# Kernel tuning notes

Measured on AMD Instinct MI355X. Metric: run time of the kernel, lower is better.

The kernel has to match this reference:

```python
import jax, jax.numpy as jnp
import numpy as np

B, C, T, H, NCLS = 512, 22, 1000, 64, 4


def setup_inputs() -> dict:
    key = jax.random.key(0)
    ks = jax.random.split(key, 8)
    s_ih = 1.0 / np.sqrt(H)
    x = jax.random.normal(ks[0], (B, C, T), dtype=jnp.float32)
    # PyTorch LSTM params: gate order [i, f, g, o], each of size H
    W_ih = jax.random.uniform(ks[1], (4 * H, C), minval=-s_ih, maxval=s_ih, dtype=jnp.float32)
    W_hh = jax.random.uniform(ks[2], (4 * H, H), minval=-s_ih, maxval=s_ih, dtype=jnp.float32)
    b_ih = jax.random.uniform(ks[3], (4 * H,), minval=-s_ih, maxval=s_ih, dtype=jnp.float32)
    b_hh = jax.random.uniform(ks[4], (4 * H,), minval=-s_ih, maxval=s_ih, dtype=jnp.float32)
    s_fc = 1.0 / np.sqrt(H * T)
    W_fc = jax.random.uniform(ks[5], (NCLS, H * T), minval=-s_fc, maxval=s_fc, dtype=jnp.float32)
    b_fc = jax.random.uniform(ks[6], (NCLS,), minval=-s_fc, maxval=s_fc, dtype=jnp.float32)
    return {"x": x, "W_ih": W_ih, "W_hh": W_hh, "b_ih": b_ih, "b_hh": b_hh,
            "W_fc": W_fc, "b_fc": b_fc}


def _lstm(xs, W_ih, W_hh, b_ih, b_hh):
    # xs: [B, T, C] -> outputs [B, T, H]
    b = xs.shape[0]
    # precompute input projections for all timesteps: [T, B, 4H]
    x_proj = jnp.einsum('btc,gc->tbg', xs, W_ih) + (b_ih + b_hh)
    h0 = jnp.zeros((b, W_hh.shape[1]), xs.dtype)
    c0 = jnp.zeros_like(h0)

    def step(carry, xp):
        h, c = carry
        gates = xp + h @ W_hh.T  # [B, 4H]
        i, f, g, o = jnp.split(gates, 4, axis=-1)
        i = jax.nn.sigmoid(i)
        f = jax.nn.sigmoid(f)
        g = jnp.tanh(g)
        o = jax.nn.sigmoid(o)
        c = f * c + i * g
        h = o * jnp.tanh(c)
        return (h, c), h

    _, hs = jax.lax.scan(step, (h0, c0), x_proj)  # hs: [T, B, H]
    return jnp.transpose(hs, (1, 0, 2))  # [B, T, H]


def reference(x, W_ih, W_hh, b_ih, b_hh, W_fc, b_fc):
    xs = jnp.transpose(x, (0, 2, 1))  # [B, T, C]  (permute(0,2,1))
    hs = _lstm(xs, W_ih, W_hh, b_ih, b_hh)  # [B, T, H]
    flat = hs.reshape(hs.shape[0], -1)  # [B, T*H], time-major per row
    logits = flat @ W_fc.T + b_fc  # [B, 4]
    return jax.nn.softmax(logits, axis=1)
```

## Files before the change

### kernel.cpp

```cpp
#include <hip/hip_runtime.h>

#define BB   512
#define CC   22
#define TT   1000
#define HH   64
#define NCLS 4
#define TC   250
#define NCHUNK (TT / TC)
#define XROW 12

typedef _Float16 f16;
typedef __attribute__((ext_vector_type(2))) _Float16 h2;

__device__ __forceinline__ float sigm(float x) {
    return 1.0f / (1.0f + __expf(-x));
}
__device__ __forceinline__ float tanh_(float x) {
    float e = __expf(-2.0f * fabsf(x));
    float r = (1.0f - e) / (1.0f + e);
    return copysignf(r, x);
}

__device__ __forceinline__ h2 u2h(unsigned u) {
    union { unsigned u; h2 h; } c; c.u = u; return c.h;
}
__device__ __forceinline__ unsigned h2u(h2 h) {
    union { unsigned u; h2 h; } c; c.h = h; return c.u;
}

__global__
__attribute__((amdgpu_flat_work_group_size(64, 64), amdgpu_waves_per_eu(1, 1)))
void lstm_wave(
    const float* __restrict__ x,
    const float* __restrict__ W_ih,
    const float* __restrict__ W_hh,
    const float* __restrict__ b_ih,
    const float* __restrict__ b_hh,
    const float* __restrict__ W_fc,
    const float* __restrict__ b_fc,
    float* __restrict__ out)
{
    __shared__ __align__(16) h2  xs[TC][XROW];
    __shared__ __align__(16) f16 hbuf[HH];

    const int lane = threadIdx.x;
    const int r    = blockIdx.x;

    unsigned whh[4][32];
    unsigned wih[4][11];
    float bias[4];
    #pragma unroll
    for (int g = 0; g < 4; ++g) {
        const int row = g * HH + lane;
        const float* wr = W_hh + row * HH;
        #pragma unroll
        for (int k = 0; k < 32; ++k)
            whh[g][k] = h2u(h2{(f16)wr[2 * k], (f16)wr[2 * k + 1]});
        const float* wi = W_ih + row * CC;
        #pragma unroll
        for (int k = 0; k < 11; ++k)
            wih[g][k] = h2u(h2{(f16)wi[2 * k], (f16)wi[2 * k + 1]});
        bias[g] = b_ih[row] + b_hh[row];
    }

    hbuf[lane] = (f16)0.0f;
    float c = 0.0f;
    float fc0 = 0.f, fc1 = 0.f, fc2 = 0.f, fc3 = 0.f;
    const float* p0 = W_fc + 0 * (TT * HH) + lane;
    const float* p1 = W_fc + 1 * (TT * HH) + lane;
    const float* p2 = W_fc + 2 * (TT * HH) + lane;
    const float* p3 = W_fc + 3 * (TT * HH) + lane;
    const float* xrow = x + (size_t)r * (CC * TT);

    for (int chunk = 0; chunk < NCHUNK; ++chunk) {
        for (int tb = 0; tb < TC; tb += 64) {
            const int t = tb + lane;
            if (t < TC) {
                const float* gx = xrow + chunk * TC + t;
                union { h2 h[XROW]; uint4 q[3]; } U;
                #pragma unroll
                for (int k = 0; k < 11; ++k)
                    U.h[k] = h2{(f16)gx[(2 * k) * TT], (f16)gx[(2 * k + 1) * TT]};
                U.h[11] = h2{(f16)0.0f, (f16)0.0f};
                uint4* dst = (uint4*)&xs[t][0];
                dst[0] = U.q[0]; dst[1] = U.q[1]; dst[2] = U.q[2];
            }
        }

        for (int tt = 0; tt < TC; ++tt) {
            union { uint4 q[8]; h2 h[32]; } H;
            const uint4* hr = (const uint4*)hbuf;
            #pragma unroll
            for (int i = 0; i < 8; ++i) H.q[i] = hr[i];

            union { uint4 q[3]; h2 h[XROW]; } X;
            const uint4* xr = (const uint4*)&xs[tt][0];
            X.q[0] = xr[0]; X.q[1] = xr[1]; X.q[2] = xr[2];

            float w0 = *p0, w1 = *p1, w2 = *p2, w3 = *p3;
            p0 += HH; p1 += HH; p2 += HH; p3 += HH;

            float a0 = bias[0], a1 = bias[1], a2 = bias[2], a3 = bias[3];
            #pragma unroll
            for (int k = 0; k < 11; ++k) {
                a0 = __builtin_amdgcn_fdot2(X.h[k], u2h(wih[0][k]), a0, false);
                a1 = __builtin_amdgcn_fdot2(X.h[k], u2h(wih[1][k]), a1, false);
                a2 = __builtin_amdgcn_fdot2(X.h[k], u2h(wih[2][k]), a2, false);
                a3 = __builtin_amdgcn_fdot2(X.h[k], u2h(wih[3][k]), a3, false);
            }
            #pragma unroll
            for (int k = 0; k < 32; ++k) {
                a0 = __builtin_amdgcn_fdot2(H.h[k], u2h(whh[0][k]), a0, false);
                a1 = __builtin_amdgcn_fdot2(H.h[k], u2h(whh[1][k]), a1, false);
                a2 = __builtin_amdgcn_fdot2(H.h[k], u2h(whh[2][k]), a2, false);
                a3 = __builtin_amdgcn_fdot2(H.h[k], u2h(whh[3][k]), a3, false);
            }

            float iv = sigm(a0), fv = sigm(a1), gv = tanh_(a2), ov = sigm(a3);
            c = fv * c + iv * gv;
            float h = ov * tanh_(c);

            fc0 += h * w0; fc1 += h * w1; fc2 += h * w2; fc3 += h * w3;

            hbuf[lane] = (f16)h;
        }
    }

    #pragma unroll
    for (int off = 32; off; off >>= 1) {
        fc0 += __shfl_down(fc0, off);
        fc1 += __shfl_down(fc1, off);
        fc2 += __shfl_down(fc2, off);
        fc3 += __shfl_down(fc3, off);
    }
    if (lane == 0) {
        float l0 = fc0 + b_fc[0], l1 = fc1 + b_fc[1];
        float l2 = fc2 + b_fc[2], l3 = fc3 + b_fc[3];
        float m  = fmaxf(fmaxf(l0, l1), fmaxf(l2, l3));
        float e0 = __expf(l0 - m), e1 = __expf(l1 - m);
        float e2 = __expf(l2 - m), e3 = __expf(l3 - m);
        float s  = e0 + e1 + e2 + e3;
        float4 o; o.x = e0 / s; o.y = e1 / s; o.z = e2 / s; o.w = e3 / s;
        *(float4*)(out + r * NCLS) = o;
    }
}

extern "C" void kernel_launch(void* const* d_in, const int* in_sizes, int n_in,
                              void* d_out, int out_size, void* d_ws, size_t ws_size,
                              hipStream_t stream) {
    const float* x    = (const float*)d_in[0];
    const float* W_ih = (const float*)d_in[1];
    const float* W_hh = (const float*)d_in[2];
    const float* b_ih = (const float*)d_in[3];
    const float* b_hh = (const float*)d_in[4];
    const float* W_fc = (const float*)d_in[5];
    const float* b_fc = (const float*)d_in[6];
    float* out = (float*)d_out;

    lstm_wave<<<BB, 64, 0, stream>>>(x, W_ih, W_hh, b_ih, b_hh, W_fc, b_fc, out);
}
```

Measured before the change: 696.7 us.

## Use MFMA for LSTM recurrence and split FC+softmax into separate kernel

Replaces per-lane fdot2 gate computation with 16x16x32 f16 MFMA ops over weights held in registers, with x padded to 32 channels. Hidden states are buffered in an LDS ring and flushed to a global workspace. A second kernel then performs the FC projection and softmax. This removes the per-step W_fc loads from the serial loop but adds large global write/read traffic, and MFMA work is padded, with only 16 of 64 lane outputs used.

```diff
diff --git a/kernel.cpp b/kernel.cpp
--- a/kernel.cpp
+++ b/kernel.cpp
@@ -5,137 +5,173 @@
 #define TT   1000
 #define HH   64
 #define NCLS 4
-#define TC   250
+#define TC   200
 #define NCHUNK (TT / TC)
-#define XROW 12
+#define RING 40
 
 typedef _Float16 f16;
-typedef __attribute__((ext_vector_type(2))) _Float16 h2;
+typedef __attribute__((ext_vector_type(8))) _Float16 f16x8;
+typedef __attribute__((ext_vector_type(4))) float    f32x4;
 
-__device__ __forceinline__ float sigm(float x) {
-    return 1.0f / (1.0f + __expf(-x));
-}
+union F8U { f16x8 v; uint4 u; f16 h[8]; };
+
+__device__ __forceinline__ float sigm(float x) { return 1.0f / (1.0f + __expf(-x)); }
 __device__ __forceinline__ float tanh_(float x) {
     float e = __expf(-2.0f * fabsf(x));
     float r = (1.0f - e) / (1.0f + e);
     return copysignf(r, x);
 }
 
-__device__ __forceinline__ h2 u2h(unsigned u) {
-    union { unsigned u; h2 h; } c; c.u = u; return c.h;
-}
-__device__ __forceinline__ unsigned h2u(h2 h) {
-    union { unsigned u; h2 h; } c; c.h = h; return c.u;
-}
-
 __global__
 __attribute__((amdgpu_flat_work_group_size(64, 64), amdgpu_waves_per_eu(1, 1)))
-void lstm_wave(
+void lstm_mfma1(
     const float* __restrict__ x,
     const float* __restrict__ W_ih,
     const float* __restrict__ W_hh,
     const float* __restrict__ b_ih,
     const float* __restrict__ b_hh,
+    f16* __restrict__ hglob)
+{
+    __shared__ __align__(16) f16 xs[TC * 32];
+    __shared__ __align__(16) f16 hring[RING * HH];
+
+    const int lane = threadIdx.x;
+    const int q    = lane >> 4;
+    const int c    = lane & 15;
+    const int r    = blockIdx.x;
+
+    f16x8 Bw0[16], Bw1[16], Bw2[16];
+    float bias_s[16];
+    #pragma unroll
+    for (int n = 0; n < 16; ++n) {
+        const int g = 16 * n + c;
+        F8U a, b, cc;
+        const float* wr = W_hh + g * HH + 8 * q;
+        #pragma unroll
+        for (int j = 0; j < 8; ++j) { a.h[j] = (f16)wr[j]; b.h[j] = (f16)wr[32 + j]; }
+        #pragma unroll
+        for (int j = 0; j < 8; ++j) {
+            const int k = 8 * q + j;
+            cc.h[j] = (k < CC) ? (f16)W_ih[g * CC + k] : (f16)0.f;
+        }
+        Bw0[n] = a.v; Bw1[n] = b.v; Bw2[n] = cc.v;
+        bias_s[n] = b_ih[g] + b_hh[g];
+    }
+
+    if (lane < 16) {
+        #pragma unroll
+        for (int j = 0; j < 4; ++j) hring[(RING - 1) * HH + 16 * j + c] = (f16)0.f;
+    }
+    float cst[4] = {0.f, 0.f, 0.f, 0.f};
+    const float* xrow = x + (size_t)r * (CC * TT);
+    f16* hout = hglob + (size_t)r * (TT * HH);
+    int sprev = RING - 1, scur = 0;
+
+    for (int chunk = 0; chunk < NCHUNK; ++chunk) {
+        for (int t0 = 0; t0 < TC; t0 += 64) {
+            const int t = t0 + lane;
+            if (t < TC) {
+                const float* gx = xrow + chunk * TC + t;
+                F8U u[4];
+                #pragma unroll
+                for (int k = 0; k < 32; ++k)
+                    u[k >> 3].h[k & 7] = (k < CC) ? (f16)gx[k * TT] : (f16)0.f;
+                uint4* dst = (uint4*)&xs[t * 32];
+                dst[0] = u[0].u; dst[1] = u[1].u; dst[2] = u[2].u; dst[3] = u[3].u;
+            }
+        }
+
+        for (int tt = 0; tt < TC; ++tt) {
+            F8U Ax;  Ax.u  = *(const uint4*)&xs[tt * 32 + 8 * q];
+            F8U Ah0; Ah0.u = *(const uint4*)&hring[sprev * HH + 8 * q];
+            F8U Ah1; Ah1.u = *(const uint4*)&hring[sprev * HH + 32 + 8 * q];
+
+            const f32x4 z = {0.f, 0.f, 0.f, 0.f};
+            f32x4 acc[16];
+            #pragma unroll
+            for (int n = 0; n < 16; ++n)
+                acc[n] = __builtin_amdgcn_mfma_f32_16x16x32_f16(Ax.v, Bw2[n], z, 0, 0, 0);
+            #pragma unroll
+            for (int n = 0; n < 16; ++n)
+                acc[n] = __builtin_amdgcn_mfma_f32_16x16x32_f16(Ah0.v, Bw0[n], acc[n], 0, 0, 0);
+            #pragma unroll
+            for (int n = 0; n < 16; ++n)
+                acc[n] = __builtin_amdgcn_mfma_f32_16x16x32_f16(Ah1.v, Bw1[n], acc[n], 0, 0, 0);
+
+            #pragma unroll
+            for (int j = 0; j < 4; ++j) {
+                float iv = sigm (acc[j][0]      + bias_s[j]);
+                float fv = sigm (acc[4 + j][0]  + bias_s[4 + j]);
+                float gv = tanh_(acc[8 + j][0]  + bias_s[8 + j]);
+                float ov = sigm (acc[12 + j][0] + bias_s[12 + j]);
+                cst[j] = fv * cst[j] + iv * gv;
+                float h = ov * tanh_(cst[j]);
+                if (lane < 16) hring[scur * HH + 16 * j + c] = (f16)h;
+            }
+
+            if (scur == RING - 1) {
+                const int t0g = chunk * TC + tt - (RING - 1);
+                #pragma unroll
+                for (int j = 0; j < 5; ++j) {
+                    uint4 v = *(const uint4*)&hring[512 * j + 8 * lane];
+                    *(uint4*)&hout[(size_t)t0g * HH + 512 * j + 8 * lane] = v;
+                }
+            }
+            sprev = scur;
+            scur  = (scur + 1 == RING) ? 0 : scur + 1;
+        }
+    }
+}
+
+__global__ __launch_bounds__(256) void fc_softmax(
+    const f16*  __restrict__ hglob,
     const float* __restrict__ W_fc,
     const float* __restrict__ b_fc,
     float* __restrict__ out)
 {
-    __shared__ __align__(16) h2  xs[TC][XROW];
-    __shared__ __align__(16) f16 hbuf[HH];
+    const int w    = threadIdx.x >> 6;
+    const int lane = threadIdx.x & 63;
+    const int r    = blockIdx.x * 4 + w;
 
-    const int lane = threadIdx.x;
-    const int r    = blockIdx.x;
+    const f16* hr = hglob + (size_t)r * (TT * HH);
+    float a0 = 0.f, a1 = 0.f, a2 = 0.f, a3 = 0.f;
 
-    unsigned whh[4][32];
-    unsigned wih[4][11];
-    float bias[4];
-    #pragma unroll
-    for (int g = 0; g < 4; ++g) {
-        const int row = g * HH + lane;
-        const float* wr = W_hh + row * HH;
+    for (int i = 0; i < (TT * HH) / 512; ++i) {
+        const int k = i * 512 + lane * 8;
+        F8U hv; hv.u = *(const uint4*)&hr[k];
+        float hf[8];
         #pragma unroll
-        for (int k = 0; k < 32; ++k)
-            whh[g][k] = h2u(h2{(f16)wr[2 * k], (f16)wr[2 * k + 1]});
-        const float* wi = W_ih + row * CC;
-        #pragma unroll
-        for (int k = 0; k < 11; ++k)
-            wih[g][k] = h2u(h2{(f16)wi[2 * k], (f16)wi[2 * k + 1]});
-        bias[g] = b_ih[row] + b_hh[row];
-    }
+        for (int j = 0; j < 8; ++j) hf[j] = (float)hv.h[j];
 
-    hbuf[lane] = (f16)0.0f;
-    float c = 0.0f;
-    float fc0 = 0.f, fc1 = 0.f, fc2 = 0.f, fc3 = 0.f;
-    const float* p0 = W_fc + 0 * (TT * HH) + lane;
-    const float* p1 = W_fc + 1 * (TT * HH) + lane;
-    const float* p2 = W_fc + 2 * (TT * HH) + lane;
-    const float* p3 = W_fc + 3 * (TT * HH) + lane;
-    const float* xrow = x + (size_t)r * (CC * TT);
+        const float* w0 = W_fc + 0 * (TT * HH) + k;
+        const float* w1 = W_fc + 1 * (TT * HH) + k;
+        const float* w2 = W_fc + 2 * (TT * HH) + k;
+        const float* w3 = W_fc + 3 * (TT * HH) + k;
+        float4 v0a = *(const float4*)w0, v0b = *(const float4*)(w0 + 4);
+        float4 v1a = *(const float4*)w1, v1b = *(const float4*)(w1 + 4);
+        float4 v2a = *(const float4*)w2, v2b = *(const float4*)(w2 + 4);
+        float4 v3a = *(const float4*)w3, v3b = *(const float4*)(w3 + 4);
 
-    for (int chunk = 0; chunk < NCHUNK; ++chunk) {
-        for (int tb = 0; tb < TC; tb += 64) {
-            const int t = tb + lane;
-            if (t < TC) {
-                const float* gx = xrow + chunk * TC + t;
-                union { h2 h[XROW]; uint4 q[3]; } U;
-                #pragma unroll
-                for (int k = 0; k < 11; ++k)
-                    U.h[k] = h2{(f16)gx[(2 * k) * TT], (f16)gx[(2 * k + 1) * TT]};
-                U.h[11] = h2{(f16)0.0f, (f16)0.0f};
-                uint4* dst = (uint4*)&xs[t][0];
-                dst[0] = U.q[0]; dst[1] = U.q[1]; dst[2] = U.q[2];
-            }
-        }
-
-        for (int tt = 0; tt < TC; ++tt) {
-            union { uint4 q[8]; h2 h[32]; } H;
-            const uint4* hr = (const uint4*)hbuf;
-            #pragma unroll
-            for (int i = 0; i < 8; ++i) H.q[i] = hr[i];
-
-            union { uint4 q[3]; h2 h[XROW]; } X;
-            const uint4* xr = (const uint4*)&xs[tt][0];
-            X.q[0] = xr[0]; X.q[1] = xr[1]; X.q[2] = xr[2];
-
-            float w0 = *p0, w1 = *p1, w2 = *p2, w3 = *p3;
-            p0 += HH; p1 += HH; p2 += HH; p3 += HH;
-
-            float a0 = bias[0], a1 = bias[1], a2 = bias[2], a3 = bias[3];
-            #pragma unroll
-            for (int k = 0; k < 11; ++k) {
-                a0 = __builtin_amdgcn_fdot2(X.h[k], u2h(wih[0][k]), a0, false);
-                a1 = __builtin_amdgcn_fdot2(X.h[k], u2h(wih[1][k]), a1, false);
-                a2 = __builtin_amdgcn_fdot2(X.h[k], u2h(wih[2][k]), a2, false);
-                a3 = __builtin_amdgcn_fdot2(X.h[k], u2h(wih[3][k]), a3, false);
-            }
-            #pragma unroll
-            for (int k = 0; k < 32; ++k) {
-                a0 = __builtin_amdgcn_fdot2(H.h[k], u2h(whh[0][k]), a0, false);
-                a1 = __builtin_amdgcn_fdot2(H.h[k], u2h(whh[1][k]), a1, false);
-                a2 = __builtin_amdgcn_fdot2(H.h[k], u2h(whh[2][k]), a2, false);
-                a3 = __builtin_amdgcn_fdot2(H.h[k], u2h(whh[3][k]), a3, false);
-            }
-
-            float iv = sigm(a0), fv = sigm(a1), gv = tanh_(a2), ov = sigm(a3);
-            c = fv * c + iv * gv;
-            float h = ov * tanh_(c);
-
-            fc0 += h * w0; fc1 += h * w1; fc2 += h * w2; fc3 += h * w3;
-
-            hbuf[lane] = (f16)h;
-        }
+        a0 += hf[0]*v0a.x + hf[1]*v0a.y + hf[2]*v0a.z + hf[3]*v0a.w
+            + hf[4]*v0b.x + hf[5]*v0b.y + hf[6]*v0b.z + hf[7]*v0b.w;
+        a1 += hf[0]*v1a.x + hf[1]*v1a.y + hf[2]*v1a.z + hf[3]*v1a.w
+            + hf[4]*v1b.x + hf[5]*v1b.y + hf[6]*v1b.z + hf[7]*v1b.w;
+        a2 += hf[0]*v2a.x + hf[1]*v2a.y + hf[2]*v2a.z + hf[3]*v2a.w
+            + hf[4]*v2b.x + hf[5]*v2b.y + hf[6]*v2b.z + hf[7]*v2b.w;
+        a3 += hf[0]*v3a.x + hf[1]*v3a.y + hf[2]*v3a.z + hf[3]*v3a.w
+            + hf[4]*v3b.x + hf[5]*v3b.y + hf[6]*v3b.z + hf[7]*v3b.w;
     }
 
     #pragma unroll
     for (int off = 32; off; off >>= 1) {
-        fc0 += __shfl_down(fc0, off);
-        fc1 += __shfl_down(fc1, off);
-        fc2 += __shfl_down(fc2, off);
-        fc3 += __shfl_down(fc3, off);
+        a0 += __shfl_down(a0, off);
+        a1 += __shfl_down(a1, off);
+        a2 += __shfl_down(a2, off);
+        a3 += __shfl_down(a3, off);
     }
     if (lane == 0) {
-        float l0 = fc0 + b_fc[0], l1 = fc1 + b_fc[1];
-        float l2 = fc2 + b_fc[2], l3 = fc3 + b_fc[3];
+        float l0 = a0 + b_fc[0], l1 = a1 + b_fc[1];
+        float l2 = a2 + b_fc[2], l3 = a3 + b_fc[3];
         float m  = fmaxf(fmaxf(l0, l1), fmaxf(l2, l3));
         float e0 = __expf(l0 - m), e1 = __expf(l1 - m);
         float e2 = __expf(l2 - m), e3 = __expf(l3 - m);
@@ -156,6 +192,8 @@
     const float* W_fc = (const float*)d_in[5];
     const float* b_fc = (const float*)d_in[6];
     float* out = (float*)d_out;
+    f16*  hglob = (f16*)d_ws;
 
-    lstm_wave<<<BB, 64, 0, stream>>>(x, W_ih, W_hh, b_ih, b_hh, W_fc, b_fc, out);
+    lstm_mfma1<<<BB, 64, 0, stream>>>(x, W_ih, W_hh, b_ih, b_hh, hglob);
+    fc_softmax<<<BB / 4, 256, 0, stream>>>(hglob, W_fc, b_fc, out);
 }
```

After: 1.348 ms. +93.5%, slower.

## Split FC into separate kernel, move W_ih to LDS, split h loads

Applied to the files above, without the earlier changes.

Moves the final FC reduction out of the recurrent kernel: each step writes h in fp16 to a workspace, and a second kernel computes logits and softmax for 16 rows per block. W_ih weights go from registers into shared memory, laid out in 16-byte chunks, to relieve register pressure in the recurrence. The h vector is now read in two halves, so the second half loads while the first half's dot products run. This removes the per-step global W_fc loads from the serial critical path. In exchange it adds a 64 MB-scale fp16 global write and re-read, plus extra LDS loads every step.

```diff
diff --git a/kernel.cpp b/kernel.cpp
--- a/kernel.cpp
+++ b/kernel.cpp
@@ -7,141 +7,231 @@
 #define NCLS 4
 #define TC   250
 #define NCHUNK (TT / TC)
-#define XROW 12
+
+#define OFF_H   0
+#define OFF_WT  32
+#define OFF_XS  (32 + 3072)
+#define SMEM_DW (32 + 3072 + 3000)
 
 typedef _Float16 f16;
 typedef __attribute__((ext_vector_type(2))) _Float16 h2;
 
-__device__ __forceinline__ float sigm(float x) {
-    return 1.0f / (1.0f + __expf(-x));
-}
+union PU { unsigned u; h2 h; };
+union QU { uint4 q; unsigned u[4]; f16 h[8]; };
+
+__device__ __forceinline__ float sigm(float x) { return 1.0f / (1.0f + __expf(-x)); }
 __device__ __forceinline__ float tanh_(float x) {
     float e = __expf(-2.0f * fabsf(x));
     float r = (1.0f - e) / (1.0f + e);
     return copysignf(r, x);
 }
-
-__device__ __forceinline__ h2 u2h(unsigned u) {
-    union { unsigned u; h2 h; } c; c.u = u; return c.h;
-}
-__device__ __forceinline__ unsigned h2u(h2 h) {
-    union { unsigned u; h2 h; } c; c.h = h; return c.u;
-}
+__device__ __forceinline__ h2 u2h(unsigned u) { PU p; p.u = u; return p.h; }
 
 __global__
 __attribute__((amdgpu_flat_work_group_size(64, 64), amdgpu_waves_per_eu(1, 1)))
-void lstm_wave(
+void lstm_row(
     const float* __restrict__ x,
     const float* __restrict__ W_ih,
     const float* __restrict__ W_hh,
     const float* __restrict__ b_ih,
     const float* __restrict__ b_hh,
-    const float* __restrict__ W_fc,
-    const float* __restrict__ b_fc,
-    float* __restrict__ out)
+    f16* __restrict__ hglob)
 {
-    __shared__ __align__(16) h2  xs[TC][XROW];
-    __shared__ __align__(16) f16 hbuf[HH];
+    __shared__ __align__(16) unsigned smem[SMEM_DW];
 
     const int lane = threadIdx.x;
     const int r    = blockIdx.x;
 
     unsigned whh[4][32];
-    unsigned wih[4][11];
     float bias[4];
     #pragma unroll
     for (int g = 0; g < 4; ++g) {
         const int row = g * HH + lane;
         const float* wr = W_hh + row * HH;
         #pragma unroll
-        for (int k = 0; k < 32; ++k)
-            whh[g][k] = h2u(h2{(f16)wr[2 * k], (f16)wr[2 * k + 1]});
-        const float* wi = W_ih + row * CC;
-        #pragma unroll
-        for (int k = 0; k < 11; ++k)
-            wih[g][k] = h2u(h2{(f16)wi[2 * k], (f16)wi[2 * k + 1]});
+        for (int k = 0; k < 32; ++k) {
+            PU p; p.h = h2{(f16)wr[2 * k], (f16)wr[2 * k + 1]};
+            whh[g][k] = p.u;
+        }
         bias[g] = b_ih[row] + b_hh[row];
     }
 
-    hbuf[lane] = (f16)0.0f;
-    float c = 0.0f;
-    float fc0 = 0.f, fc1 = 0.f, fc2 = 0.f, fc3 = 0.f;
-    const float* p0 = W_fc + 0 * (TT * HH) + lane;
-    const float* p1 = W_fc + 1 * (TT * HH) + lane;
-    const float* p2 = W_fc + 2 * (TT * HH) + lane;
-    const float* p3 = W_fc + 3 * (TT * HH) + lane;
+    #pragma unroll
+    for (int G = 0; G < 4; ++G) {
+        const int g = G * 64 + lane;
+        const float* wi = W_ih + g * CC;
+        #pragma unroll
+        for (int k4 = 0; k4 < 3; ++k4) {
+            QU q;
+            #pragma unroll
+            for (int j = 0; j < 4; ++j) {
+                const int c0 = 8 * k4 + 2 * j;
+                float lo = (c0     < CC) ? wi[c0]     : 0.f;
+                float hi = (c0 + 1 < CC) ? wi[c0 + 1] : 0.f;
+                PU p; p.h = h2{(f16)lo, (f16)hi};
+                q.u[j] = p.u;
+            }
+            *(uint4*)&smem[OFF_WT + (k4 * 256 + g) * 4] = q.q;
+        }
+    }
+
+    ((f16*)smem)[lane] = (f16)0.f;
+
+    float c = 0.f;
     const float* xrow = x + (size_t)r * (CC * TT);
+    f16* hout = hglob + (size_t)r * (TT * HH) + lane;
 
     for (int chunk = 0; chunk < NCHUNK; ++chunk) {
-        for (int tb = 0; tb < TC; tb += 64) {
-            const int t = tb + lane;
+        for (int t0 = 0; t0 < TC; t0 += 64) {
+            const int t = t0 + lane;
             if (t < TC) {
                 const float* gx = xrow + chunk * TC + t;
-                union { h2 h[XROW]; uint4 q[3]; } U;
-                #pragma unroll
-                for (int k = 0; k < 11; ++k)
-                    U.h[k] = h2{(f16)gx[(2 * k) * TT], (f16)gx[(2 * k + 1) * TT]};
-                U.h[11] = h2{(f16)0.0f, (f16)0.0f};
-                uint4* dst = (uint4*)&xs[t][0];
-                dst[0] = U.q[0]; dst[1] = U.q[1]; dst[2] = U.q[2];
+                QU A, Bq, Cq;
+                #pragma unroll
+                for (int j = 0; j < 4; ++j) {
+                    PU p; p.h = h2{(f16)gx[(2*j)*TT], (f16)gx[(2*j+1)*TT]};
+                    A.u[j] = p.u;
+                }
+                #pragma unroll
+                for (int j = 0; j < 4; ++j) {
+                    PU p; p.h = h2{(f16)gx[(8+2*j)*TT], (f16)gx[(9+2*j)*TT]};
+                    Bq.u[j] = p.u;
+                }
+                #pragma unroll
+                for (int j = 0; j < 3; ++j) {
+                    PU p; p.h = h2{(f16)gx[(16+2*j)*TT], (f16)gx[(17+2*j)*TT]};
+                    Cq.u[j] = p.u;
+                }
+                Cq.u[3] = 0u;
+                uint4* dst = (uint4*)&smem[OFF_XS + t * 12];
+                dst[0] = A.q; dst[1] = Bq.q; dst[2] = Cq.q;
             }
         }
 
         for (int tt = 0; tt < TC; ++tt) {
-            union { uint4 q[8]; h2 h[32]; } H;
-            const uint4* hr = (const uint4*)hbuf;
-            #pragma unroll
-            for (int i = 0; i < 8; ++i) H.q[i] = hr[i];
-
-            union { uint4 q[3]; h2 h[XROW]; } X;
-            const uint4* xr = (const uint4*)&xs[tt][0];
-            X.q[0] = xr[0]; X.q[1] = xr[1]; X.q[2] = xr[2];
-
-            float w0 = *p0, w1 = *p1, w2 = *p2, w3 = *p3;
-            p0 += HH; p1 += HH; p2 += HH; p3 += HH;
+            union { uint4 q[4]; unsigned u[16]; } Ha, Hb;
+            const uint4* hp = (const uint4*)&smem[OFF_H];
+            Ha.q[0] = hp[0]; Ha.q[1] = hp[1]; Ha.q[2] = hp[2]; Ha.q[3] = hp[3];
+
+            union { uint4 q[3]; unsigned u[12]; } X;
+            const uint4* xp = (const uint4*)&smem[OFF_XS + tt * 12];
+            X.q[0] = xp[0]; X.q[1] = xp[1]; X.q[2] = xp[2];
 
             float a0 = bias[0], a1 = bias[1], a2 = bias[2], a3 = bias[3];
-            #pragma unroll
-            for (int k = 0; k < 11; ++k) {
-                a0 = __builtin_amdgcn_fdot2(X.h[k], u2h(wih[0][k]), a0, false);
-                a1 = __builtin_amdgcn_fdot2(X.h[k], u2h(wih[1][k]), a1, false);
-                a2 = __builtin_amdgcn_fdot2(X.h[k], u2h(wih[2][k]), a2, false);
-                a3 = __builtin_amdgcn_fdot2(X.h[k], u2h(wih[3][k]), a3, false);
-            }
-            #pragma unroll
-            for (int k = 0; k < 32; ++k) {
-                a0 = __builtin_amdgcn_fdot2(H.h[k], u2h(whh[0][k]), a0, false);
-                a1 = __builtin_amdgcn_fdot2(H.h[k], u2h(whh[1][k]), a1, false);
-                a2 = __builtin_amdgcn_fdot2(H.h[k], u2h(whh[2][k]), a2, false);
-                a3 = __builtin_amdgcn_fdot2(H.h[k], u2h(whh[3][k]), a3, false);
+            {
+                uint4 wf0, wf1, wf2;
+                #pragma unroll
+                for (int G = 0; G < 4; ++G) {
+                    wf0 = *(const uint4*)&smem[OFF_WT + (0 * 256 + G * 64 + lane) * 4];
+                    wf1 = *(const uint4*)&smem[OFF_WT + (1 * 256 + G * 64 + lane) * 4];
+                    wf2 = *(const uint4*)&smem[OFF_WT + (2 * 256 + G * 64 + lane) * 4];
+                    QU w0; w0.q = wf0;  QU w1; w1.q = wf1;  QU w2; w2.q = wf2;
+                    float a = (G == 0) ? a0 : (G == 1) ? a1 : (G == 2) ? a2 : a3;
+                    #pragma unroll
+                    for (int j = 0; j < 4; ++j) a = __builtin_amdgcn_fdot2(u2h(X.u[j]),     u2h(w0.u[j]), a, false);
+                    #pragma unroll
+                    for (int j = 0; j < 4; ++j) a = __builtin_amdgcn_fdot2(u2h(X.u[4 + j]), u2h(w1.u[j]), a, false);
+                    #pragma unroll
+                    for (int j = 0; j < 4; ++j) a = __builtin_amdgcn_fdot2(u2h(X.u[8 + j]), u2h(w2.u[j]), a, false);
+                    if (G == 0) a0 = a; else if (G == 1) a1 = a; else if (G == 2) a2 = a; else a3 = a;
+                }
+            }
+
+            #pragma unroll
+            for (int k = 0; k < 16; ++k) {
+                h2 hv = u2h(Ha.u[k]);
+                a0 = __builtin_amdgcn_fdot2(hv, u2h(whh[0][k]), a0, false);
+                a1 = __builtin_amdgcn_fdot2(hv, u2h(whh[1][k]), a1, false);
+                a2 = __builtin_amdgcn_fdot2(hv, u2h(whh[2][k]), a2, false);
+                a3 = __builtin_amdgcn_fdot2(hv, u2h(whh[3][k]), a3, false);
+            }
+            Hb.q[0] = hp[4]; Hb.q[1] = hp[5]; Hb.q[2] = hp[6]; Hb.q[3] = hp[7];
+            #pragma unroll
+            for (int k = 0; k < 16; ++k) {
+                h2 hv = u2h(Hb.u[k]);
+                a0 = __builtin_amdgcn_fdot2(hv, u2h(whh[0][16 + k]), a0, false);
+                a1 = __builtin_amdgcn_fdot2(hv, u2h(whh[1][16 + k]), a1, false);
+                a2 = __builtin_amdgcn_fdot2(hv, u2h(whh[2][16 + k]), a2, false);
+                a3 = __builtin_amdgcn_fdot2(hv, u2h(whh[3][16 + k]), a3, false);
             }
 
             float iv = sigm(a0), fv = sigm(a1), gv = tanh_(a2), ov = sigm(a3);
             c = fv * c + iv * gv;
             float h = ov * tanh_(c);
 
-            fc0 += h * w0; fc1 += h * w1; fc2 += h * w2; fc3 += h * w3;
-
-            hbuf[lane] = (f16)h;
+            f16 hf = (f16)h;
+            ((f16*)smem)[lane] = hf;
+            hout[(chunk * TC + tt) * HH] = hf;
+        }
+    }
+}
+
+__global__ __launch_bounds__(256) void fc_softmax16(
+    const f16*  __restrict__ hglob,
+    const float* __restrict__ W_fc,
+    const float* __restrict__ b_fc,
+    float* __restrict__ out)
+{
+    const int w    = threadIdx.x >> 6;
+    const int lane = threadIdx.x & 63;
+    const int r0   = blockIdx.x * 16 + w * 4;
+
+    const f16* hr0 = hglob + (size_t)(r0 + 0) * (TT * HH);
+    const f16* hr1 = hglob + (size_t)(r0 + 1) * (TT * HH);
+    const f16* hr2 = hglob + (size_t)(r0 + 2) * (TT * HH);
+    const f16* hr3 = hglob + (size_t)(r0 + 3) * (TT * HH);
+
+    float acc[4][4] = {{0.f}};
+
+    for (int i = 0; i < (TT * HH) / 512; ++i) {
+        const int k = i * 512 + lane * 8;
+
+        float4 wa[4], wb[4];
+        #pragma unroll
+        for (int cl = 0; cl < 4; ++cl) {
+            const float* wp = W_fc + (size_t)cl * (TT * HH) + k;
+            wa[cl] = *(const float4*)wp;
+            wb[cl] = *(const float4*)(wp + 4);
+        }
+        QU hv[4];
+        hv[0].q = *(const uint4*)&hr0[k];
+        hv[1].q = *(const uint4*)&hr1[k];
+        hv[2].q = *(const uint4*)&hr2[k];
+        hv[3].q = *(const uint4*)&hr3[k];
+
+        #pragma unroll
+        for (int rr = 0; rr < 4; ++rr) {
+            float hf[8];
+            #pragma unroll
+            for (int j = 0; j < 8; ++j) hf[j] = (float)hv[rr].h[j];
+            #pragma unroll
+            for (int cl = 0; cl < 4; ++cl) {
+                acc[rr][cl] += hf[0]*wa[cl].x + hf[1]*wa[cl].y + hf[2]*wa[cl].z + hf[3]*wa[cl].w
+                             + hf[4]*wb[cl].x + hf[5]*wb[cl].y + hf[6]*wb[cl].z + hf[7]*wb[cl].w;
+            }
         }
     }
 
     #pragma unroll
-    for (int off = 32; off; off >>= 1) {
-        fc0 += __shfl_down(fc0, off);
-        fc1 += __shfl_down(fc1, off);
-        fc2 += __shfl_down(fc2, off);
-        fc3 += __shfl_down(fc3, off);
-    }
+    for (int rr = 0; rr < 4; ++rr)
+        #pragma unroll
+        for (int cl = 0; cl < 4; ++cl)
+            #pragma unroll
+            for (int off = 32; off; off >>= 1)
+                acc[rr][cl] += __shfl_down(acc[rr][cl], off);
+
     if (lane == 0) {
-        float l0 = fc0 + b_fc[0], l1 = fc1 + b_fc[1];
-        float l2 = fc2 + b_fc[2], l3 = fc3 + b_fc[3];
-        float m  = fmaxf(fmaxf(l0, l1), fmaxf(l2, l3));
-        float e0 = __expf(l0 - m), e1 = __expf(l1 - m);
-        float e2 = __expf(l2 - m), e3 = __expf(l3 - m);
-        float s  = e0 + e1 + e2 + e3;
-        float4 o; o.x = e0 / s; o.y = e1 / s; o.z = e2 / s; o.w = e3 / s;
-        *(float4*)(out + r * NCLS) = o;
+        #pragma unroll
+        for (int rr = 0; rr < 4; ++rr) {
+            float l0 = acc[rr][0] + b_fc[0], l1 = acc[rr][1] + b_fc[1];
+            float l2 = acc[rr][2] + b_fc[2], l3 = acc[rr][3] + b_fc[3];
+            float m  = fmaxf(fmaxf(l0, l1), fmaxf(l2, l3));
+            float e0 = __expf(l0 - m), e1 = __expf(l1 - m);
+            float e2 = __expf(l2 - m), e3 = __expf(l3 - m);
+            float s  = e0 + e1 + e2 + e3;
+            float4 o; o.x = e0 / s; o.y = e1 / s; o.z = e2 / s; o.w = e3 / s;
+            *(float4*)(out + (r0 + rr) * NCLS) = o;
+        }
     }
 }
 
@@ -156,6 +246,8 @@
     const float* W_fc = (const float*)d_in[5];
     const float* b_fc = (const float*)d_in[6];
     float* out = (float*)d_out;
-
-    lstm_wave<<<BB, 64, 0, stream>>>(x, W_ih, W_hh, b_ih, b_hh, W_fc, b_fc, out);
-}
+    f16*  hglob = (f16*)d_ws;
+
+    lstm_row<<<BB, 64, 0, stream>>>(x, W_ih, W_hh, b_ih, b_hh, hglob);
+    fc_softmax16<<<BB / 16, 256, 0, stream>>>(hglob, W_fc, b_fc, out);
+}
```

Result: slower. 765.9 us (+9.9%).
